# Optimization experiments

Hardware: AMD Instinct MI355X
Metric: run time of the kernel (lower is better)

## Reference

```python
import jax, jax.numpy as jnp
import numpy as np

BATCH, N_REC, D_HIDDEN = 8192, 1024, 2048
RMIN, RMAX = 0.4, 0.99

def _half_glorot(key, shape):
    # VarianceScaling(scale=1/2, fan_avg, uniform): limit = sqrt(3*scale/fan_avg)
    fan_avg = (shape[0] + shape[1]) / 2.0
    limit = np.sqrt(1.5 / fan_avg)
    return jax.random.uniform(key, shape, jnp.float32, -limit, limit)

def setup_inputs() -> dict:
    key = jax.random.key(0)
    ks = jax.random.split(key, 11)
    inputs = jax.random.normal(ks[0], (BATCH, N_REC), jnp.float32)
    state_re = jax.random.normal(ks[1], (BATCH, D_HIDDEN), jnp.float32)
    state_im = jax.random.normal(ks[2], (BATCH, D_HIDDEN), jnp.float32)
    C_re = _half_glorot(ks[3], (D_HIDDEN, N_REC))
    C_im = _half_glorot(ks[4], (D_HIDDEN, N_REC))
    B_re = _half_glorot(ks[5], (N_REC, D_HIDDEN))
    B_im = _half_glorot(ks[6], (N_REC, D_HIDDEN))
    D = jax.random.normal(ks[7], (N_REC,), jnp.float32)
    numax = float(np.log(-np.log(RMIN)))
    numin = float(np.log(-np.log(RMAX)))
    nu = jax.random.uniform(ks[8], (D_HIDDEN,), jnp.float32, numin, numax)
    theta = jax.random.uniform(ks[9], (D_HIDDEN,), jnp.float32, 0.0, 3.14 / 10)
    # gamma initialized to sqrt(1 - |lambda|^2), |lambda| = exp(-exp(nu))
    gamma = jnp.sqrt(1.0 - jnp.exp(-2.0 * jnp.exp(nu)))
    return {"inputs": inputs, "state_re": state_re, "state_im": state_im,
            "B_re": B_re, "B_im": B_im, "C_re": C_re, "C_im": C_im,
            "D": D, "nu": nu, "theta": theta, "gamma": gamma}

def reference(inputs, state_re, state_im, B_re, B_im, C_re, C_im, D, nu, theta, gamma):
    # lambda = exp(-exp(nu) + i*theta), diagonal complex recurrence
    lam = (jnp.exp(-jnp.exp(nu)) * jnp.exp(1j * theta)).astype(jnp.complex64)  # [H]
    x = (state_re + 1j * state_im).astype(jnp.complex64)  # [B,H]
    B = (B_re + 1j * B_im).astype(jnp.complex64)          # [N,H]
    C = (C_re + 1j * C_im).astype(jnp.complex64)          # [H,N]
    u_ = inputs.astype(jnp.complex64)
    new_u = gamma.astype(jnp.complex64) * (u_ @ B)        # [B,H]
    x_ = x * lam + new_u                                  # diag matmul == elementwise
    y = jnp.real(x_ @ C) + D * inputs                     # [B,N]
    return y, jnp.real(x_), jnp.imag(x_)
```

## Files before the change

kernel.cpp:

```cpp
#include <hip/hip_runtime.h>
#include <hip/hip_bf16.h>

typedef __bf16 bf16;
typedef __attribute__((ext_vector_type(8))) __bf16 bf16x8;
typedef __attribute__((ext_vector_type(4))) float floatx4;

#define BATCH 8192
#define NREC  1024
#define DHID  2048

#define GLOBAL_AS __attribute__((address_space(1)))
#define LDS_AS    __attribute__((address_space(3)))

__device__ __forceinline__ bf16 to_bf16(float f) { return (bf16)f; }

__device__ __forceinline__ void async16(const void* g, void* l) {
  __builtin_amdgcn_global_load_lds((const GLOBAL_AS unsigned int*)g,
                                   (LDS_AS unsigned int*)l, 16, 0, 0);
}


__global__ void lam_kernel(const float* __restrict__ nu, const float* __restrict__ theta,
                           float* __restrict__ lamRe, float* __restrict__ lamIm) {
  int h = blockIdx.x * blockDim.x + threadIdx.x;
  if (h < DHID) {
    float t = expf(-expf(nu[h]));
    lamRe[h] = t * cosf(theta[h]);
    lamIm[h] = t * sinf(theta[h]);
  }
}

__global__ void convert_kernel(const float* __restrict__ src, bf16* __restrict__ dst) {
  int idx = blockIdx.x * blockDim.x + threadIdx.x;
  float4 v = reinterpret_cast<const float4*>(src)[idx];
  ushort4 pk;
  pk.x = __builtin_bit_cast(unsigned short, to_bf16(v.x));
  pk.y = __builtin_bit_cast(unsigned short, to_bf16(v.y));
  pk.z = __builtin_bit_cast(unsigned short, to_bf16(v.z));
  pk.w = __builtin_bit_cast(unsigned short, to_bf16(v.w));
  *reinterpret_cast<ushort4*>(dst + (size_t)idx * 4) = pk;
}

__global__ void transpose_kernel(const float* __restrict__ src, int C,
                                 bf16* __restrict__ dst, int dstStride, float scale) {
  __shared__ float tile[32][33];
  int c0 = blockIdx.x * 32, r0 = blockIdx.y * 32;
  #pragma unroll
  for (int i = 0; i < 32; i += 8) {
    tile[threadIdx.y + i][threadIdx.x] =
        src[(size_t)(r0 + threadIdx.y + i) * C + c0 + threadIdx.x];
  }
  __syncthreads();
  #pragma unroll
  for (int i = 0; i < 32; i += 8) {
    int c = c0 + threadIdx.y + i;
    dst[(size_t)c * dstStride + r0 + threadIdx.x] =
        to_bf16(scale * tile[threadIdx.x][threadIdx.y + i]);
  }
}


__global__ __launch_bounds__(256, 2) void gemm1_kernel(
    const bf16* __restrict__ A,
    const bf16* __restrict__ BreT,
    const bf16* __restrict__ BimT,
    const float* __restrict__ state_re,
    const float* __restrict__ state_im,
    const float* __restrict__ gamma,
    const float* __restrict__ lamRe,
    const float* __restrict__ lamIm,
    float* __restrict__ xre_out,
    float* __restrict__ xim_out,
    bf16* __restrict__ Xcat)
{
  __shared__ __align__(16) bf16 Alds[128 * 32];
  __shared__ __align__(16) bf16 BreLds[128 * 32];
  __shared__ __align__(16) bf16 BimLds[128 * 32];

  const int tid   = threadIdx.x;
  const int mBase = blockIdx.y * 128;
  const int hBase = blockIdx.x * 128;
  const int lane  = tid & 63;
  const int wave  = tid >> 6;
  const int wr    = (wave >> 1) * 64;
  const int wc    = (wave & 1) * 64;
  const int m16   = lane & 15;
  const int q     = lane >> 4;

  floatx4 zero = {0.f, 0.f, 0.f, 0.f};
  floatx4 accRe[4][4], accIm[4][4];
  #pragma unroll
  for (int i = 0; i < 4; ++i)
    #pragma unroll
    for (int j = 0; j < 4; ++j) { accRe[i][j] = zero; accIm[i][j] = zero; }

  const int row0 = tid >> 2;
  const int seg  = (tid & 3) * 8;
  const int wbase = wave * 512;

  for (int kt = 0; kt < 1024; kt += 32) {
    #pragma unroll
    for (int p = 0; p < 2; ++p) {
      const int row = row0 + p * 64;
      const size_t aoff = (size_t)(mBase + row) * 1024 + kt + seg;
      const size_t boff = (size_t)(hBase + row) * 1024 + kt + seg;
      async16(&A[aoff],    &Alds[p * 2048 + wbase]);
      async16(&BreT[boff], &BreLds[p * 2048 + wbase]);
      async16(&BimT[boff], &BimLds[p * 2048 + wbase]);
    }
    __syncthreads();

    bf16x8 aF[4], brF[4], biF[4];
    #pragma unroll
    for (int i = 0; i < 4; ++i)
      aF[i] = *reinterpret_cast<const bf16x8*>(&Alds[(wr + i * 16 + m16) * 32 + q * 8]);
    #pragma unroll
    for (int j = 0; j < 4; ++j) {
      brF[j] = *reinterpret_cast<const bf16x8*>(&BreLds[(wc + j * 16 + m16) * 32 + q * 8]);
      biF[j] = *reinterpret_cast<const bf16x8*>(&BimLds[(wc + j * 16 + m16) * 32 + q * 8]);
    }
    #pragma unroll
    for (int i = 0; i < 4; ++i)
      #pragma unroll
      for (int j = 0; j < 4; ++j) {
        accRe[i][j] = __builtin_amdgcn_mfma_f32_16x16x32_bf16(aF[i], brF[j], accRe[i][j], 0, 0, 0);
        accIm[i][j] = __builtin_amdgcn_mfma_f32_16x16x32_bf16(aF[i], biF[j], accIm[i][j], 0, 0, 0);
      }
    __syncthreads();
  }

  #pragma unroll
  for (int j = 0; j < 4; ++j) {
    const int h  = hBase + wc + j * 16 + m16;
    const float g  = gamma[h];
    const float lr = lamRe[h];
    const float li = lamIm[h];
    #pragma unroll
    for (int i = 0; i < 4; ++i) {
      #pragma unroll
      for (int r = 0; r < 4; ++r) {
        const int row = mBase + wr + i * 16 + q * 4 + r;
        const size_t off = (size_t)row * DHID + h;
        const float ur = g * accRe[i][j][r];
        const float ui = g * accIm[i][j][r];
        const float sr = state_re[off];
        const float si = state_im[off];
        const float xr = sr * lr - si * li + ur;
        const float xi = sr * li + si * lr + ui;
        xre_out[off] = xr;
        xim_out[off] = xi;
        const size_t xoff = (size_t)row * (2 * DHID) + h;
        Xcat[xoff]        = to_bf16(xr);
        Xcat[xoff + DHID] = to_bf16(xi);
      }
    }
  }
}


__global__ __launch_bounds__(256, 2) void gemm2_kernel(
    const bf16* __restrict__ Xcat,
    const bf16* __restrict__ CcatT,
    const float* __restrict__ Dvec,
    const float* __restrict__ inputs,
    float* __restrict__ y)
{
  __shared__ __align__(16) bf16 Alds[128 * 32];
  __shared__ __align__(16) bf16 Blds[128 * 32];

  const int tid   = threadIdx.x;
  const int mBase = blockIdx.y * 128;
  const int nBase = blockIdx.x * 128;
  const int lane  = tid & 63;
  const int wave  = tid >> 6;
  const int wr    = (wave >> 1) * 64;
  const int wc    = (wave & 1) * 64;
  const int m16   = lane & 15;
  const int q     = lane >> 4;

  floatx4 zero = {0.f, 0.f, 0.f, 0.f};
  floatx4 acc[4][4];
  #pragma unroll
  for (int i = 0; i < 4; ++i)
    #pragma unroll
    for (int j = 0; j < 4; ++j) acc[i][j] = zero;

  const int row0 = tid >> 2;
  const int seg  = (tid & 3) * 8;
  const int wbase = wave * 512;

  for (int kt = 0; kt < 4096; kt += 32) {
    #pragma unroll
    for (int p = 0; p < 2; ++p) {
      const int row = row0 + p * 64;
      const size_t aoff = (size_t)(mBase + row) * 4096 + kt + seg;
      const size_t boff = (size_t)(nBase + row) * 4096 + kt + seg;
      async16(&Xcat[aoff],  &Alds[p * 2048 + wbase]);
      async16(&CcatT[boff], &Blds[p * 2048 + wbase]);
    }
    __syncthreads();

    bf16x8 aF[4], bF[4];
    #pragma unroll
    for (int i = 0; i < 4; ++i)
      aF[i] = *reinterpret_cast<const bf16x8*>(&Alds[(wr + i * 16 + m16) * 32 + q * 8]);
    #pragma unroll
    for (int j = 0; j < 4; ++j)
      bF[j] = *reinterpret_cast<const bf16x8*>(&Blds[(wc + j * 16 + m16) * 32 + q * 8]);

    #pragma unroll
    for (int i = 0; i < 4; ++i)
      #pragma unroll
      for (int j = 0; j < 4; ++j)
        acc[i][j] = __builtin_amdgcn_mfma_f32_16x16x32_bf16(aF[i], bF[j], acc[i][j], 0, 0, 0);
    __syncthreads();
  }

  #pragma unroll
  for (int j = 0; j < 4; ++j) {
    const int n = nBase + wc + j * 16 + m16;
    const float dv = Dvec[n];
    #pragma unroll
    for (int i = 0; i < 4; ++i) {
      #pragma unroll
      for (int r = 0; r < 4; ++r) {
        const int row = mBase + wr + i * 16 + q * 4 + r;
        const size_t idx = (size_t)row * NREC + n;
        y[idx] = acc[i][j][r] + dv * inputs[idx];
      }
    }
  }
}


extern "C" void kernel_launch(void* const* d_in, const int* in_sizes, int n_in,
                              void* d_out, int out_size, void* d_ws, size_t ws_size,
                              hipStream_t stream) {
  (void)in_sizes; (void)n_in; (void)out_size; (void)ws_size;

  const float* inputs   = (const float*)d_in[0];
  const float* state_re = (const float*)d_in[1];
  const float* state_im = (const float*)d_in[2];
  const float* B_re     = (const float*)d_in[3];
  const float* B_im     = (const float*)d_in[4];
  const float* C_re     = (const float*)d_in[5];
  const float* C_im     = (const float*)d_in[6];
  const float* Dvec     = (const float*)d_in[7];
  const float* nu       = (const float*)d_in[8];
  const float* theta    = (const float*)d_in[9];
  const float* gamma    = (const float*)d_in[10];

  float* out     = (float*)d_out;
  float* y_out   = out;
  float* xre_out = out + (size_t)BATCH * NREC;
  float* xim_out = xre_out + (size_t)BATCH * DHID;

  char* ws = (char*)d_ws;
  bf16*  A1    = (bf16*)(ws + 0);
  bf16*  BreT  = (bf16*)(ws + 16777216);
  bf16*  BimT  = (bf16*)(ws + 20971520);
  bf16*  CcatT = (bf16*)(ws + 25165824);
  bf16*  Xcat  = (bf16*)(ws + 33554432);
  float* lamRe = (float*)(ws + 100663296);
  float* lamIm = (float*)(ws + 100671488);

  lam_kernel<<<dim3(DHID / 256), dim3(256), 0, stream>>>(nu, theta, lamRe, lamIm);
  convert_kernel<<<dim3((BATCH * NREC) / 1024), dim3(256), 0, stream>>>(inputs, A1);

  dim3 tb(32, 8);
  transpose_kernel<<<dim3(2048 / 32, 1024 / 32), tb, 0, stream>>>(B_re, 2048, BreT, 1024, 1.0f);
  transpose_kernel<<<dim3(2048 / 32, 1024 / 32), tb, 0, stream>>>(B_im, 2048, BimT, 1024, 1.0f);
  transpose_kernel<<<dim3(1024 / 32, 2048 / 32), tb, 0, stream>>>(C_re, 1024, CcatT, 4096, 1.0f);
  transpose_kernel<<<dim3(1024 / 32, 2048 / 32), tb, 0, stream>>>(C_im, 1024, CcatT + 2048, 4096, -1.0f);

  gemm1_kernel<<<dim3(DHID / 128, BATCH / 128), dim3(256), 0, stream>>>(
      A1, BreT, BimT, state_re, state_im, gamma, lamRe, lamIm, xre_out, xim_out, Xcat);

  gemm2_kernel<<<dim3(NREC / 128, BATCH / 128), dim3(256), 0, stream>>>(
      Xcat, CcatT, Dvec, inputs, y_out);
}
```

Before: 640.6 us.

## Double-buffer LDS tiles and XOR-swizzle fragment layout in both GEMMs

Both GEMM kernels now keep two LDS buffers per operand and issue the async global-to-LDS loads for the next K tile before computing on the current one, leaving one barrier per iteration instead of two. LDS chunk positions are also XOR-swizzled by row, both when staging and when reading fragments, to reduce bank conflicts on the 16-byte fragment reads. The cost is double the LDS footprint, which may reduce occupancy at 2 blocks per CU. There is also a correctness risk: the loop relies on __syncthreads to wait on async LDS loads that are still in flight.

```diff
diff --git a/kernel.cpp b/kernel.cpp
--- a/kernel.cpp
+++ b/kernel.cpp
@@ -17,6 +17,11 @@
 __device__ __forceinline__ void async16(const void* g, void* l) {
   __builtin_amdgcn_global_load_lds((const GLOBAL_AS unsigned int*)g,
                                    (LDS_AS unsigned int*)l, 16, 0, 0);
+}
+
+__device__ __forceinline__ bf16x8 ldsFrag(const bf16* buf, int row, int q) {
+  const int s = (q ^ ((row >> 1) & 3)) * 8;
+  return *reinterpret_cast<const bf16x8*>(&buf[row * 32 + s]);
 }
 
 
@@ -73,9 +78,9 @@
     float* __restrict__ xim_out,
     bf16* __restrict__ Xcat)
 {
-  __shared__ __align__(16) bf16 Alds[128 * 32];
-  __shared__ __align__(16) bf16 BreLds[128 * 32];
-  __shared__ __align__(16) bf16 BimLds[128 * 32];
+  __shared__ __align__(16) bf16 Alds[2][128 * 32];
+  __shared__ __align__(16) bf16 BreLds[2][128 * 32];
+  __shared__ __align__(16) bf16 BimLds[2][128 * 32];
 
   const int tid   = threadIdx.x;
   const int mBase = blockIdx.y * 128;
@@ -95,29 +100,30 @@
     for (int j = 0; j < 4; ++j) { accRe[i][j] = zero; accIm[i][j] = zero; }
 
   const int row0 = tid >> 2;
-  const int seg  = (tid & 3) * 8;
   const int wbase = wave * 512;
 
-  for (int kt = 0; kt < 1024; kt += 32) {
+  auto stage = [&](int buf, int kt) {
     #pragma unroll
     for (int p = 0; p < 2; ++p) {
-      const int row = row0 + p * 64;
-      const size_t aoff = (size_t)(mBase + row) * 1024 + kt + seg;
-      const size_t boff = (size_t)(hBase + row) * 1024 + kt + seg;
-      async16(&A[aoff],    &Alds[p * 2048 + wbase]);
-      async16(&BreT[boff], &BreLds[p * 2048 + wbase]);
-      async16(&BimT[boff], &BimLds[p * 2048 + wbase]);
-    }
-    __syncthreads();
-
+      const int r  = row0 + p * 64;
+      const int ss = ((tid & 3) ^ ((r >> 1) & 3)) * 8;
+      const size_t aoff = (size_t)(mBase + r) * 1024 + kt + ss;
+      const size_t boff = (size_t)(hBase + r) * 1024 + kt + ss;
+      async16(&A[aoff],    &Alds[buf][p * 2048 + wbase]);
+      async16(&BreT[boff], &BreLds[buf][p * 2048 + wbase]);
+      async16(&BimT[boff], &BimLds[buf][p * 2048 + wbase]);
+    }
+  };
+
+  auto computeTile = [&](int buf) {
     bf16x8 aF[4], brF[4], biF[4];
     #pragma unroll
     for (int i = 0; i < 4; ++i)
-      aF[i] = *reinterpret_cast<const bf16x8*>(&Alds[(wr + i * 16 + m16) * 32 + q * 8]);
+      aF[i] = ldsFrag(Alds[buf], wr + i * 16 + m16, q);
     #pragma unroll
     for (int j = 0; j < 4; ++j) {
-      brF[j] = *reinterpret_cast<const bf16x8*>(&BreLds[(wc + j * 16 + m16) * 32 + q * 8]);
-      biF[j] = *reinterpret_cast<const bf16x8*>(&BimLds[(wc + j * 16 + m16) * 32 + q * 8]);
+      brF[j] = ldsFrag(BreLds[buf], wc + j * 16 + m16, q);
+      biF[j] = ldsFrag(BimLds[buf], wc + j * 16 + m16, q);
     }
     #pragma unroll
     for (int i = 0; i < 4; ++i)
@@ -126,8 +132,18 @@
         accRe[i][j] = __builtin_amdgcn_mfma_f32_16x16x32_bf16(aF[i], brF[j], accRe[i][j], 0, 0, 0);
         accIm[i][j] = __builtin_amdgcn_mfma_f32_16x16x32_bf16(aF[i], biF[j], accIm[i][j], 0, 0, 0);
       }
+  };
+
+  stage(0, 0);
+  __syncthreads();
+  int cur = 0;
+  for (int kt = 32; kt < 1024; kt += 32) {
+    stage(cur ^ 1, kt);
+    computeTile(cur);
     __syncthreads();
-  }
+    cur ^= 1;
+  }
+  computeTile(cur);
 
   #pragma unroll
   for (int j = 0; j < 4; ++j) {
@@ -165,8 +181,8 @@
     const float* __restrict__ inputs,
     float* __restrict__ y)
 {
-  __shared__ __align__(16) bf16 Alds[128 * 32];
-  __shared__ __align__(16) bf16 Blds[128 * 32];
+  __shared__ __align__(16) bf16 Alds[2][128 * 32];
+  __shared__ __align__(16) bf16 Blds[2][128 * 32];
 
   const int tid   = threadIdx.x;
   const int mBase = blockIdx.y * 128;
@@ -186,35 +202,45 @@
     for (int j = 0; j < 4; ++j) acc[i][j] = zero;
 
   const int row0 = tid >> 2;
-  const int seg  = (tid & 3) * 8;
   const int wbase = wave * 512;
 
-  for (int kt = 0; kt < 4096; kt += 32) {
+  auto stage = [&](int buf, int kt) {
     #pragma unroll
     for (int p = 0; p < 2; ++p) {
-      const int row = row0 + p * 64;
-      const size_t aoff = (size_t)(mBase + row) * 4096 + kt + seg;
-      const size_t boff = (size_t)(nBase + row) * 4096 + kt + seg;
-      async16(&Xcat[aoff],  &Alds[p * 2048 + wbase]);
-      async16(&CcatT[boff], &Blds[p * 2048 + wbase]);
-    }
-    __syncthreads();
-
+      const int r  = row0 + p * 64;
+      const int ss = ((tid & 3) ^ ((r >> 1) & 3)) * 8;
+      const size_t aoff = (size_t)(mBase + r) * 4096 + kt + ss;
+      const size_t boff = (size_t)(nBase + r) * 4096 + kt + ss;
+      async16(&Xcat[aoff],  &Alds[buf][p * 2048 + wbase]);
+      async16(&CcatT[boff], &Blds[buf][p * 2048 + wbase]);
+    }
+  };
+
+  auto computeTile = [&](int buf) {
     bf16x8 aF[4], bF[4];
     #pragma unroll
     for (int i = 0; i < 4; ++i)
-      aF[i] = *reinterpret_cast<const bf16x8*>(&Alds[(wr + i * 16 + m16) * 32 + q * 8]);
+      aF[i] = ldsFrag(Alds[buf], wr + i * 16 + m16, q);
     #pragma unroll
     for (int j = 0; j < 4; ++j)
-      bF[j] = *reinterpret_cast<const bf16x8*>(&Blds[(wc + j * 16 + m16) * 32 + q * 8]);
-
+      bF[j] = ldsFrag(Blds[buf], wc + j * 16 + m16, q);
     #pragma unroll
     for (int i = 0; i < 4; ++i)
       #pragma unroll
       for (int j = 0; j < 4; ++j)
         acc[i][j] = __builtin_amdgcn_mfma_f32_16x16x32_bf16(aF[i], bF[j], acc[i][j], 0, 0, 0);
+  };
+
+  stage(0, 0);
+  __syncthreads();
+  int cur = 0;
+  for (int kt = 32; kt < 4096; kt += 32) {
+    stage(cur ^ 1, kt);
+    computeTile(cur);
     __syncthreads();
-  }
+    cur ^= 1;
+  }
+  computeTile(cur);
 
   #pragma unroll
   for (int j = 0; j < 4; ++j) {
```

Measured after the change: 638.6 us. No clear change (-0.3%).

## Restructure both GEMMs with larger tiles, double-buffered swizzled LDS and interleaved B

Applied to the files above, without the earlier changes.

Rewrites both GEMM kernels to use 512-thread blocks with larger tiles (256x256 for gemm1, 128x256 for gemm2) and K-step 64. The LDS tiles are double-buffered and XOR-swizzled. The main loop is a hand-scheduled ping-pong that overlaps async global-to-LDS loads with MFMA phases, using explicit barriers, vmcnt/lgkmcnt waits and setprio. B_re/B_im are interleaved into one concatenated matrix, so gemm1 runs a single real GEMM over 2*DHID columns and the epilogue picks the real or imaginary path by column parity. The goal is less global/LDS traffic per FLOP, fewer bank conflicts and hidden load latency, at the cost of many barriers and a fragile hand-written schedule whose waits must match the loads exactly.

```diff
diff --git a/kernel.cpp b/kernel.cpp
--- a/kernel.cpp
+++ b/kernel.cpp
@@ -18,6 +18,21 @@
   __builtin_amdgcn_global_load_lds((const GLOBAL_AS unsigned int*)g,
                                    (LDS_AS unsigned int*)l, 16, 0, 0);
 }
+
+#define BAR()                                 \
+  do {                                        \
+    asm volatile("" ::: "memory");            \
+    __builtin_amdgcn_s_barrier();             \
+    asm volatile("" ::: "memory");            \
+  } while (0)
+
+#define LGKM0()                                            \
+  do {                                                     \
+    asm volatile("s_waitcnt lgkmcnt(0)" ::: "memory");     \
+    __builtin_amdgcn_sched_barrier(0);                     \
+  } while (0)
+
+#define VMW(N) asm volatile("s_waitcnt vmcnt(" #N ")" ::: "memory")
 
 
 __global__ void lam_kernel(const float* __restrict__ nu, const float* __restrict__ theta,
@@ -42,7 +57,8 @@
 }
 
 __global__ void transpose_kernel(const float* __restrict__ src, int C,
-                                 bf16* __restrict__ dst, int dstStride, float scale) {
+                                 bf16* __restrict__ dst, int dstStride, float scale,
+                                 int rowMul, int rowAdd) {
   __shared__ float tile[32][33];
   int c0 = blockIdx.x * 32, r0 = blockIdx.y * 32;
   #pragma unroll
@@ -54,16 +70,53 @@
   #pragma unroll
   for (int i = 0; i < 32; i += 8) {
     int c = c0 + threadIdx.y + i;
-    dst[(size_t)c * dstStride + r0 + threadIdx.x] =
+    dst[((size_t)c * rowMul + rowAdd) * dstStride + r0 + threadIdx.x] =
         to_bf16(scale * tile[threadIdx.x][threadIdx.y + i]);
   }
 }
 
 
-__global__ __launch_bounds__(256, 2) void gemm1_kernel(
+#define G1_RDA(BUF, MH)                                                        \
+  {                                                                            \
+    _Pragma("unroll") for (int f = 0; f < 4; ++f) {                            \
+      _Pragma("unroll") for (int ks = 0; ks < 2; ++ks) {                       \
+        const int row_ = wr + ((MH) * 4 + f) * 16 + m16;                       \
+        aF[f][ks] = *reinterpret_cast<const bf16x8*>(                          \
+            &Al[BUF][row_ * 64 + (((ks << 2) | q) ^ (row_ & 7)) * 8]);         \
+      }                                                                        \
+    }                                                                          \
+  }
+
+#define G1_RDB(BUF, NH)                                                        \
+  {                                                                            \
+    _Pragma("unroll") for (int g = 0; g < 2; ++g) {                            \
+      _Pragma("unroll") for (int ks = 0; ks < 2; ++ks) {                       \
+        const int row_ = wc + ((NH) * 2 + g) * 16 + m16;                       \
+        bF[NH][g][ks] = *reinterpret_cast<const bf16x8*>(                      \
+            &Bl[BUF][row_ * 64 + (((ks << 2) | q) ^ (row_ & 7)) * 8]);         \
+      }                                                                        \
+    }                                                                          \
+  }
+
+#define G1_MMA(MH, NH)                                                         \
+  {                                                                            \
+    __builtin_amdgcn_s_setprio(1);                                             \
+    _Pragma("unroll") for (int f = 0; f < 4; ++f) {                            \
+      _Pragma("unroll") for (int g = 0; g < 2; ++g) {                          \
+        _Pragma("unroll") for (int ks = 0; ks < 2; ++ks) {                     \
+          acc[(MH) * 4 + f][(NH) * 2 + g] =                                    \
+              __builtin_amdgcn_mfma_f32_16x16x32_bf16(                         \
+                  aF[f][ks], bF[NH][g][ks], acc[(MH) * 4 + f][(NH) * 2 + g],   \
+                  0, 0, 0);                                                    \
+        }                                                                      \
+      }                                                                        \
+    }                                                                          \
+    __builtin_amdgcn_s_setprio(0);                                             \
+  }
+
+__global__ __launch_bounds__(512, 2) void gemm1_kernel(
     const bf16* __restrict__ A,
-    const bf16* __restrict__ BreT,
-    const bf16* __restrict__ BimT,
+    const bf16* __restrict__ Bcat,
     const float* __restrict__ state_re,
     const float* __restrict__ state_im,
     const float* __restrict__ gamma,
@@ -73,148 +126,241 @@
     float* __restrict__ xim_out,
     bf16* __restrict__ Xcat)
 {
-  __shared__ __align__(16) bf16 Alds[128 * 32];
-  __shared__ __align__(16) bf16 BreLds[128 * 32];
-  __shared__ __align__(16) bf16 BimLds[128 * 32];
+  __shared__ __align__(16) bf16 Al[2][256 * 64];
+  __shared__ __align__(16) bf16 Bl[2][256 * 64];
 
   const int tid   = threadIdx.x;
-  const int mBase = blockIdx.y * 128;
-  const int hBase = blockIdx.x * 128;
+  const int mBase = blockIdx.y * 256;
+  const int nBase = blockIdx.x * 256;
   const int lane  = tid & 63;
   const int wave  = tid >> 6;
-  const int wr    = (wave >> 1) * 64;
-  const int wc    = (wave & 1) * 64;
+  const int wr    = (wave >> 2) * 128;
+  const int wc    = (wave & 3) * 64;
   const int m16   = lane & 15;
   const int q     = lane >> 4;
 
-  floatx4 zero = {0.f, 0.f, 0.f, 0.f};
-  floatx4 accRe[4][4], accIm[4][4];
-  #pragma unroll
-  for (int i = 0; i < 4; ++i)
-    #pragma unroll
-    for (int j = 0; j < 4; ++j) { accRe[i][j] = zero; accIm[i][j] = zero; }
-
-  const int row0 = tid >> 2;
-  const int seg  = (tid & 3) * 8;
-  const int wbase = wave * 512;
-
-  for (int kt = 0; kt < 1024; kt += 32) {
+  floatx4 acc[8][4];
+  #pragma unroll
+  for (int i = 0; i < 8; ++i)
+    #pragma unroll
+    for (int j = 0; j < 4; ++j) acc[i][j] = floatx4{0.f, 0.f, 0.f, 0.f};
+
+  bf16x8 aF[4][2];
+  bf16x8 bF[2][2][2];
+
+  auto stA = [&](int buf_, int kt, int half) {
     #pragma unroll
     for (int p = 0; p < 2; ++p) {
-      const int row = row0 + p * 64;
-      const size_t aoff = (size_t)(mBase + row) * 1024 + kt + seg;
-      const size_t boff = (size_t)(hBase + row) * 1024 + kt + seg;
-      async16(&A[aoff],    &Alds[p * 2048 + wbase]);
-      async16(&BreT[boff], &BreLds[p * 2048 + wbase]);
-      async16(&BimT[boff], &BimLds[p * 2048 + wbase]);
+      const int pos = p * 512 + tid;
+      const int r   = pos >> 3;
+      const int ss  = ((pos & 7) ^ (r & 7)) * 8;
+      const bf16* g = &A[(size_t)(mBase + half * 128 + r) * 1024 + kt * 64 + ss];
+      async16(g, &Al[buf_][half * 8192 + p * 4096 + wave * 512]);
     }
-    __syncthreads();
-
-    bf16x8 aF[4], brF[4], biF[4];
-    #pragma unroll
-    for (int i = 0; i < 4; ++i)
-      aF[i] = *reinterpret_cast<const bf16x8*>(&Alds[(wr + i * 16 + m16) * 32 + q * 8]);
-    #pragma unroll
-    for (int j = 0; j < 4; ++j) {
-      brF[j] = *reinterpret_cast<const bf16x8*>(&BreLds[(wc + j * 16 + m16) * 32 + q * 8]);
-      biF[j] = *reinterpret_cast<const bf16x8*>(&BimLds[(wc + j * 16 + m16) * 32 + q * 8]);
+  };
+  auto stB = [&](int buf_, int kt, int half) {
+    #pragma unroll
+    for (int p = 0; p < 2; ++p) {
+      const int pos = p * 512 + tid;
+      const int r   = pos >> 3;
+      const int ss  = ((pos & 7) ^ (r & 7)) * 8;
+      const bf16* g = &Bcat[(size_t)(nBase + half * 128 + r) * 1024 + kt * 64 + ss];
+      async16(g, &Bl[buf_][half * 8192 + p * 4096 + wave * 512]);
     }
-    #pragma unroll
-    for (int i = 0; i < 4; ++i)
-      #pragma unroll
-      for (int j = 0; j < 4; ++j) {
-        accRe[i][j] = __builtin_amdgcn_mfma_f32_16x16x32_bf16(aF[i], brF[j], accRe[i][j], 0, 0, 0);
-        accIm[i][j] = __builtin_amdgcn_mfma_f32_16x16x32_bf16(aF[i], biF[j], accIm[i][j], 0, 0, 0);
-      }
-    __syncthreads();
-  }
+  };
+
+  stA(0, 0, 0); stA(0, 0, 1); stB(0, 0, 0); stB(0, 0, 1);
+  stB(1, 1, 0); stB(1, 1, 1);
+  VMW(4);
+  BAR();
+
+  int kt0 = 0;
+  #pragma unroll 1
+  for (int it = 0; it < 7; ++it, kt0 += 2) {
+    G1_RDA(0, 0); G1_RDB(0, 0); stA(1, kt0 + 1, 0);
+    BAR(); LGKM0(); G1_MMA(0, 0); BAR();
+    G1_RDB(0, 1); stA(1, kt0 + 1, 1);
+    BAR(); LGKM0(); G1_MMA(0, 1); BAR();
+    G1_RDA(0, 1); stB(0, kt0 + 2, 0);
+    BAR(); LGKM0(); G1_MMA(1, 1); BAR();
+    stB(0, kt0 + 2, 1); VMW(4);
+    BAR(); G1_MMA(1, 0); BAR();
+    G1_RDA(1, 0); G1_RDB(1, 0); stA(0, kt0 + 2, 0);
+    BAR(); LGKM0(); G1_MMA(0, 0); BAR();
+    G1_RDB(1, 1); stA(0, kt0 + 2, 1);
+    BAR(); LGKM0(); G1_MMA(0, 1); BAR();
+    G1_RDA(1, 1); stB(1, kt0 + 3, 0);
+    BAR(); LGKM0(); G1_MMA(1, 1); BAR();
+    stB(1, kt0 + 3, 1); VMW(4);
+    BAR(); G1_MMA(1, 0); BAR();
+  }
+  G1_RDA(0, 0); G1_RDB(0, 0); stA(1, 15, 0);
+  BAR(); LGKM0(); G1_MMA(0, 0); BAR();
+  G1_RDB(0, 1); stA(1, 15, 1);
+  BAR(); LGKM0(); G1_MMA(0, 1); BAR();
+  G1_RDA(0, 1);
+  BAR(); LGKM0(); G1_MMA(1, 1); BAR();
+  VMW(0);
+  BAR(); G1_MMA(1, 0); BAR();
+  G1_RDA(1, 0); G1_RDB(1, 0);
+  BAR(); LGKM0(); G1_MMA(0, 0); BAR();
+  G1_RDB(1, 1);
+  BAR(); LGKM0(); G1_MMA(0, 1); BAR();
+  G1_RDA(1, 1);
+  BAR(); LGKM0(); G1_MMA(1, 1); BAR();
+  G1_MMA(1, 0);
 
   #pragma unroll
   for (int j = 0; j < 4; ++j) {
-    const int h  = hBase + wc + j * 16 + m16;
-    const float g  = gamma[h];
+    const int nn = nBase + wc + j * 16 + m16;
+    const int h  = nn >> 1;
+    const int p  = nn & 1;
+    const float gm = gamma[h];
     const float lr = lamRe[h];
     const float li = lamIm[h];
     #pragma unroll
-    for (int i = 0; i < 4; ++i) {
+    for (int i = 0; i < 8; ++i) {
       #pragma unroll
       for (int r = 0; r < 4; ++r) {
         const int row = mBase + wr + i * 16 + q * 4 + r;
         const size_t off = (size_t)row * DHID + h;
-        const float ur = g * accRe[i][j][r];
-        const float ui = g * accIm[i][j][r];
         const float sr = state_re[off];
         const float si = state_im[off];
-        const float xr = sr * lr - si * li + ur;
-        const float xi = sr * li + si * lr + ui;
-        xre_out[off] = xr;
-        xim_out[off] = xi;
-        const size_t xoff = (size_t)row * (2 * DHID) + h;
-        Xcat[xoff]        = to_bf16(xr);
-        Xcat[xoff + DHID] = to_bf16(xi);
+        const float u  = gm * acc[i][j][r];
+        const float val = p ? (sr * li + si * lr + u)
+                            : (sr * lr - si * li + u);
+        (p ? xim_out : xre_out)[off] = val;
+        Xcat[(size_t)row * (2 * DHID) + h + p * DHID] = to_bf16(val);
       }
     }
   }
 }
 
 
-__global__ __launch_bounds__(256, 2) void gemm2_kernel(
+#define G2_RDA(BUF, MH)                                                        \
+  {                                                                            \
+    _Pragma("unroll") for (int f = 0; f < 2; ++f) {                            \
+      _Pragma("unroll") for (int ks = 0; ks < 2; ++ks) {                       \
+        const int row_ = wr + ((MH) * 2 + f) * 16 + m16;                       \
+        aF[f][ks] = *reinterpret_cast<const bf16x8*>(                          \
+            &Al[BUF][row_ * 64 + (((ks << 2) | q) ^ (row_ & 7)) * 8]);         \
+      }                                                                        \
+    }                                                                          \
+  }
+
+#define G2_RDB(BUF, NH)                                                        \
+  {                                                                            \
+    _Pragma("unroll") for (int g = 0; g < 2; ++g) {                            \
+      _Pragma("unroll") for (int ks = 0; ks < 2; ++ks) {                       \
+        const int row_ = wc + ((NH) * 2 + g) * 16 + m16;                       \
+        bF[NH][g][ks] = *reinterpret_cast<const bf16x8*>(                      \
+            &Bl[BUF][row_ * 64 + (((ks << 2) | q) ^ (row_ & 7)) * 8]);         \
+      }                                                                        \
+    }                                                                          \
+  }
+
+#define G2_MMA(MH, NH)                                                         \
+  {                                                                            \
+    __builtin_amdgcn_s_setprio(1);                                             \
+    _Pragma("unroll") for (int f = 0; f < 2; ++f) {                            \
+      _Pragma("unroll") for (int g = 0; g < 2; ++g) {                          \
+        _Pragma("unroll") for (int ks = 0; ks < 2; ++ks) {                     \
+          acc[(MH) * 2 + f][(NH) * 2 + g] =                                    \
+              __builtin_amdgcn_mfma_f32_16x16x32_bf16(                         \
+                  aF[f][ks], bF[NH][g][ks], acc[(MH) * 2 + f][(NH) * 2 + g],   \
+                  0, 0, 0);                                                    \
+        }                                                                      \
+      }                                                                        \
+    }                                                                          \
+    __builtin_amdgcn_s_setprio(0);                                             \
+  }
+
+__global__ __launch_bounds__(512, 2) void gemm2_kernel(
     const bf16* __restrict__ Xcat,
     const bf16* __restrict__ CcatT,
     const float* __restrict__ Dvec,
     const float* __restrict__ inputs,
     float* __restrict__ y)
 {
-  __shared__ __align__(16) bf16 Alds[128 * 32];
-  __shared__ __align__(16) bf16 Blds[128 * 32];
+  __shared__ __align__(16) bf16 Al[2][128 * 64];
+  __shared__ __align__(16) bf16 Bl[2][256 * 64];
 
   const int tid   = threadIdx.x;
   const int mBase = blockIdx.y * 128;
-  const int nBase = blockIdx.x * 128;
+  const int nBase = blockIdx.x * 256;
   const int lane  = tid & 63;
   const int wave  = tid >> 6;
-  const int wr    = (wave >> 1) * 64;
-  const int wc    = (wave & 1) * 64;
+  const int wr    = (wave >> 2) * 64;
+  const int wc    = (wave & 3) * 64;
   const int m16   = lane & 15;
   const int q     = lane >> 4;
 
-  floatx4 zero = {0.f, 0.f, 0.f, 0.f};
   floatx4 acc[4][4];
   #pragma unroll
   for (int i = 0; i < 4; ++i)
     #pragma unroll
-    for (int j = 0; j < 4; ++j) acc[i][j] = zero;
-
-  const int row0 = tid >> 2;
-  const int seg  = (tid & 3) * 8;
-  const int wbase = wave * 512;
-
-  for (int kt = 0; kt < 4096; kt += 32) {
+    for (int j = 0; j < 4; ++j) acc[i][j] = floatx4{0.f, 0.f, 0.f, 0.f};
+
+  bf16x8 aF[2][2];
+  bf16x8 bF[2][2][2];
+
+  auto stA = [&](int buf_, int kt, int half) {
+    const int r  = tid >> 3;
+    const int ss = ((tid & 7) ^ (r & 7)) * 8;
+    const bf16* g = &Xcat[(size_t)(mBase + half * 64 + r) * 4096 + kt * 64 + ss];
+    async16(g, &Al[buf_][half * 4096 + wave * 512]);
+  };
+  auto stB = [&](int buf_, int kt, int half) {
     #pragma unroll
     for (int p = 0; p < 2; ++p) {
-      const int row = row0 + p * 64;
-      const size_t aoff = (size_t)(mBase + row) * 4096 + kt + seg;
-      const size_t boff = (size_t)(nBase + row) * 4096 + kt + seg;
-      async16(&Xcat[aoff],  &Alds[p * 2048 + wbase]);
-      async16(&CcatT[boff], &Blds[p * 2048 + wbase]);
+      const int pos = p * 512 + tid;
+      const int r   = pos >> 3;
+      const int ss  = ((pos & 7) ^ (r & 7)) * 8;
+      const bf16* g = &CcatT[(size_t)(nBase + half * 128 + r) * 4096 + kt * 64 + ss];
+      async16(g, &Bl[buf_][half * 8192 + p * 4096 + wave * 512]);
     }
-    __syncthreads();
-
-    bf16x8 aF[4], bF[4];
-    #pragma unroll
-    for (int i = 0; i < 4; ++i)
-      aF[i] = *reinterpret_cast<const bf16x8*>(&Alds[(wr + i * 16 + m16) * 32 + q * 8]);
-    #pragma unroll
-    for (int j = 0; j < 4; ++j)
-      bF[j] = *reinterpret_cast<const bf16x8*>(&Blds[(wc + j * 16 + m16) * 32 + q * 8]);
-
-    #pragma unroll
-    for (int i = 0; i < 4; ++i)
-      #pragma unroll
-      for (int j = 0; j < 4; ++j)
-        acc[i][j] = __builtin_amdgcn_mfma_f32_16x16x32_bf16(aF[i], bF[j], acc[i][j], 0, 0, 0);
-    __syncthreads();
-  }
+  };
+
+  stA(0, 0, 0); stA(0, 0, 1); stB(0, 0, 0); stB(0, 0, 1);
+  stB(1, 1, 0); stB(1, 1, 1);
+  VMW(4);
+  BAR();
+
+  int kt0 = 0;
+  #pragma unroll 1
+  for (int it = 0; it < 31; ++it, kt0 += 2) {
+    G2_RDA(0, 0); G2_RDB(0, 0); stA(1, kt0 + 1, 0);
+    BAR(); LGKM0(); G2_MMA(0, 0); BAR();
+    G2_RDB(0, 1); stA(1, kt0 + 1, 1);
+    BAR(); LGKM0(); G2_MMA(0, 1); BAR();
+    G2_RDA(0, 1); stB(0, kt0 + 2, 0);
+    BAR(); LGKM0(); G2_MMA(1, 1); BAR();
+    stB(0, kt0 + 2, 1); VMW(4);
+    BAR(); G2_MMA(1, 0); BAR();
+    G2_RDA(1, 0); G2_RDB(1, 0); stA(0, kt0 + 2, 0);
+    BAR(); LGKM0(); G2_MMA(0, 0); BAR();
+    G2_RDB(1, 1); stA(0, kt0 + 2, 1);
+    BAR(); LGKM0(); G2_MMA(0, 1); BAR();
+    G2_RDA(1, 1); stB(1, kt0 + 3, 0);
+    BAR(); LGKM0(); G2_MMA(1, 1); BAR();
+    stB(1, kt0 + 3, 1); VMW(4);
+    BAR(); G2_MMA(1, 0); BAR();
+  }
+  G2_RDA(0, 0); G2_RDB(0, 0); stA(1, 63, 0);
+  BAR(); LGKM0(); G2_MMA(0, 0); BAR();
+  G2_RDB(0, 1); stA(1, 63, 1);
+  BAR(); LGKM0(); G2_MMA(0, 1); BAR();
+  G2_RDA(0, 1);
+  BAR(); LGKM0(); G2_MMA(1, 1); BAR();
+  VMW(0);
+  BAR(); G2_MMA(1, 0); BAR();
+  G2_RDA(1, 0); G2_RDB(1, 0);
+  BAR(); LGKM0(); G2_MMA(0, 0); BAR();
+  G2_RDB(1, 1);
+  BAR(); LGKM0(); G2_MMA(0, 1); BAR();
+  G2_RDA(1, 1);
+  BAR(); LGKM0(); G2_MMA(1, 1); BAR();
+  G2_MMA(1, 0);
 
   #pragma unroll
   for (int j = 0; j < 4; ++j) {
@@ -257,8 +403,7 @@
 
   char* ws = (char*)d_ws;
   bf16*  A1    = (bf16*)(ws + 0);
-  bf16*  BreT  = (bf16*)(ws + 16777216);
-  bf16*  BimT  = (bf16*)(ws + 20971520);
+  bf16*  Bcat  = (bf16*)(ws + 16777216);
   bf16*  CcatT = (bf16*)(ws + 25165824);
   bf16*  Xcat  = (bf16*)(ws + 33554432);
   float* lamRe = (float*)(ws + 100663296);
@@ -268,14 +413,14 @@
   convert_kernel<<<dim3((BATCH * NREC) / 1024), dim3(256), 0, stream>>>(inputs, A1);
 
   dim3 tb(32, 8);
-  transpose_kernel<<<dim3(2048 / 32, 1024 / 32), tb, 0, stream>>>(B_re, 2048, BreT, 1024, 1.0f);
-  transpose_kernel<<<dim3(2048 / 32, 1024 / 32), tb, 0, stream>>>(B_im, 2048, BimT, 1024, 1.0f);
-  transpose_kernel<<<dim3(1024 / 32, 2048 / 32), tb, 0, stream>>>(C_re, 1024, CcatT, 4096, 1.0f);
-  transpose_kernel<<<dim3(1024 / 32, 2048 / 32), tb, 0, stream>>>(C_im, 1024, CcatT + 2048, 4096, -1.0f);
-
-  gemm1_kernel<<<dim3(DHID / 128, BATCH / 128), dim3(256), 0, stream>>>(
-      A1, BreT, BimT, state_re, state_im, gamma, lamRe, lamIm, xre_out, xim_out, Xcat);
-
-  gemm2_kernel<<<dim3(NREC / 128, BATCH / 128), dim3(256), 0, stream>>>(
+  transpose_kernel<<<dim3(2048 / 32, 1024 / 32), tb, 0, stream>>>(B_re, 2048, Bcat, 1024, 1.0f, 2, 0);
+  transpose_kernel<<<dim3(2048 / 32, 1024 / 32), tb, 0, stream>>>(B_im, 2048, Bcat, 1024, 1.0f, 2, 1);
+  transpose_kernel<<<dim3(1024 / 32, 2048 / 32), tb, 0, stream>>>(C_re, 1024, CcatT, 4096, 1.0f, 1, 0);
+  transpose_kernel<<<dim3(1024 / 32, 2048 / 32), tb, 0, stream>>>(C_im, 1024, CcatT + 2048, 4096, -1.0f, 1, 0);
+
+  gemm1_kernel<<<dim3(DHID * 2 / 256, BATCH / 256), dim3(512), 0, stream>>>(
+      A1, Bcat, state_re, state_im, gamma, lamRe, lamIm, xre_out, xim_out, Xcat);
+
+  gemm2_kernel<<<dim3(NREC / 256, BATCH / 128), dim3(512), 0, stream>>>(
       Xcat, CcatT, Dvec, inputs, y_out);
 }
```

New measurement: 749.3 us. +17.0%, slower.
